# Kernel tuning notes

Measured on AMD Instinct MI355X. Metric: run time of the kernel, lower is better.

Reference implementation:

```python
import math
import jax, jax.numpy as jnp
import numpy as np

D_MODEL = 1024
N_HEADS = 16
HEAD_DIM = D_MODEL // N_HEADS
FEATURE_DIM = 16
WINDOW = 64
EPS_NORM = 1e-6
EPS_DEN = 1e-6

_TRIU_I, _TRIU_J = np.triu_indices(FEATURE_DIM)

def taylor_feature_map(x):
    # x: [B,T,H,f] -> [B,T,H,1+f+f(f+1)/2]
    B, T, H, d = x.shape
    ones = jnp.ones((B, T, H, 1), dtype=x.dtype)
    outer = jnp.einsum('bthd,bthe->bthde', x, x)
    scale = jnp.full((d, d), 1.0 / math.sqrt(2), dtype=x.dtype)
    scale = scale.at[jnp.arange(d), jnp.arange(d)].set(0.5)
    outer = outer * scale
    quadratic = outer[..., _TRIU_I, _TRIU_J]
    return jnp.concatenate([ones, x, quadratic], axis=-1)

def rmsnorm(x, w):
    var = jnp.mean(x * x, axis=-1, keepdims=True)
    return x * jax.lax.rsqrt(var + EPS_NORM) * w

def setup_inputs() -> dict:
    key = jax.random.key(0)
    ks = jax.random.split(key, 9)
    B, T = 2, 2048
    std = 0.02
    return {
        'x': jax.random.normal(ks[0], (B, T, D_MODEL), jnp.float32),
        'encoder_out': jax.random.normal(ks[1], (B, T, D_MODEL), jnp.float32),
        'norm_w': jnp.ones((D_MODEL,), jnp.float32),
        'Wq': jax.random.normal(ks[2], (D_MODEL, D_MODEL), jnp.float32) * std,
        'Wkv': jax.random.normal(ks[3], (D_MODEL, 2 * D_MODEL), jnp.float32) * std,
        'Wqf': jax.random.normal(ks[4], (HEAD_DIM, FEATURE_DIM), jnp.float32) * std,
        'Wkf': jax.random.normal(ks[5], (HEAD_DIM, FEATURE_DIM), jnp.float32) * std,
        'Wwin': jax.random.normal(ks[6], (D_MODEL, 2 * D_MODEL), jnp.float32) * std,
        'Wout': jax.random.normal(ks[7], (2 * D_MODEL, D_MODEL), jnp.float32) * std,
    }

def _forward(x, encoder_out, norm_w, Wq, Wkv, Wqf, Wkf, Wwin, Wout):
    residual = x
    xn = rmsnorm(x, norm_w)
    B, T_dec, _ = xn.shape
    T_enc = encoder_out.shape[1]
    H, hd = N_HEADS, HEAD_DIM

    q = (xn @ Wq).reshape(B, T_dec, H, hd)
    kv = (encoder_out @ Wkv).reshape(B, T_enc, 2, H, hd)
    k, v = kv[:, :, 0], kv[:, :, 1]

    # Taylor linear cross-attention
    q_phi = taylor_feature_map(q @ Wqf)   # [B,T_dec,H,F]
    k_phi = taylor_feature_map(k @ Wkf)   # [B,T_enc,H,F]
    kv_state = jnp.einsum('bshf,bshd->bhfd', k_phi, v)
    k_state = k_phi.sum(axis=1)           # [B,H,F]
    linear_out = jnp.einsum('bthf,bhfd->bthd', q_phi, kv_state)
    normalizer = jnp.einsum('bthf,bhf->bth', q_phi, k_state)[..., None]
    linear_out = (linear_out / (normalizer + EPS_DEN)).reshape(B, T_dec, D_MODEL)

    # Sliding-window causal self-attention (flash window_size=(WINDOW,0))
    kv_win = (xn @ Wwin).reshape(B, T_dec, 2, H, hd)
    k_win, v_win = kv_win[:, :, 0], kv_win[:, :, 1]
    scores = jnp.einsum('bthd,bshd->bhts', q, k_win) * (1.0 / math.sqrt(hd))
    i = jnp.arange(T_dec)[:, None]
    j = jnp.arange(T_dec)[None, :]
    allowed = (j <= i) & (j >= i - WINDOW)
    scores = jnp.where(allowed, scores, jnp.finfo(scores.dtype).min)
    probs = jax.nn.softmax(scores, axis=-1)
    window_out = jnp.einsum('bhts,bshd->bthd', probs, v_win).reshape(B, T_dec, D_MODEL)

    combined = jnp.concatenate([linear_out, window_out], axis=-1)
    return residual + combined @ Wout

def reference(x, encoder_out, norm_w, Wq, Wkv, Wqf, Wkf, Wwin, Wout):
    return _forward(x, encoder_out, norm_w, Wq, Wkv, Wqf, Wkf, Wwin, Wout)
```

## Files before the change

kernel.cpp:

```cpp
#include <hip/hip_runtime.h>

#define DM 1024
#define NH 16
#define HD 64
#define FD 16
#define NF 153
#define FPAD 160
#define WIN 64
#define TSEQ 2048
#define ROWS 4096
#define KSPLIT 8
#define RS2 0.70710678118654752f

typedef unsigned short u16;
typedef __attribute__((ext_vector_type(8))) short bf16x8;
typedef __attribute__((ext_vector_type(8))) unsigned short u16x8;
typedef __attribute__((ext_vector_type(4))) unsigned short u16x4;
typedef __attribute__((ext_vector_type(4))) float f32x4;

#define GLB_AS __attribute__((address_space(1)))
#define LDS_AS __attribute__((address_space(3)))

static __device__ __forceinline__ void gload_lds16(const void* g, void* l){
  __builtin_amdgcn_global_load_lds((const GLB_AS void*)g, (LDS_AS void*)l, 16, 0, 0);
}

static __device__ __forceinline__ float bf2f(u16 u){
  unsigned v = ((unsigned)u) << 16;
  return __builtin_bit_cast(float, v);
}
static __device__ __forceinline__ u16 f2bf(float f){
  unsigned u = __builtin_bit_cast(unsigned, f);
  u += 0x7FFFu + ((u >> 16) & 1u);
  return (u16)(u >> 16);
}

static __device__ __forceinline__ void tr_tile(const float* __restrict__ in,
    u16* __restrict__ out, int K, int N, int n0, int k0, float* t, int tid){
  int tx = tid & 31, ty = tid >> 5;
  #pragma unroll
  for (int i=0;i<4;i++) t[(ty + i*8)*33 + tx] = in[(size_t)(k0 + ty + i*8)*N + n0 + tx];
  __syncthreads();
  #pragma unroll
  for (int i=0;i<4;i++) out[(size_t)(n0 + ty + i*8)*K + k0 + tx] = f2bf(t[tx*33 + ty + i*8]);
}

__global__ __launch_bounds__(256) void k_prep(const float* __restrict__ x,
    const float* __restrict__ enc, const float* __restrict__ w,
    const float* __restrict__ Wq, const float* __restrict__ Wwin,
    const float* __restrict__ Wkv, const float* __restrict__ Wout,
    const float* __restrict__ Wqf, const float* __restrict__ Wkf,
    u16* __restrict__ xn, u16* __restrict__ encb,
    u16* __restrict__ WqwT, u16* __restrict__ WkvT, u16* __restrict__ WoutT,
    u16* __restrict__ WqfT, u16* __restrict__ WkfT){
  __shared__ float t[32*33];
  int bx = blockIdx.x, tid = threadIdx.x;
  if (bx < ROWS){
    int row = bx;
    const float4* xr = (const float4*)(x + (size_t)row*DM);
    float4 a = xr[tid];
    float ss = a.x*a.x + a.y*a.y + a.z*a.z + a.w*a.w;
    #pragma unroll
    for (int m=1;m<64;m<<=1) ss += __shfl_xor(ss, m);
    __shared__ float red[4];
    if ((tid&63)==0) red[tid>>6] = ss;
    __syncthreads();
    float tot = red[0]+red[1]+red[2]+red[3];
    float rs = rsqrtf(tot*(1.0f/DM) + 1e-6f);
    float4 wv = ((const float4*)w)[tid];
    u16x4 o;
    o[0]=f2bf(a.x*rs*wv.x); o[1]=f2bf(a.y*rs*wv.y);
    o[2]=f2bf(a.z*rs*wv.z); o[3]=f2bf(a.w*rs*wv.w);
    ((u16x4*)(xn + (size_t)row*DM))[tid] = o;
  } else if (bx < 2*ROWS){
    int row = bx - ROWS;
    float4 a = ((const float4*)(enc + (size_t)row*DM))[tid];
    u16x4 o;
    o[0]=f2bf(a.x); o[1]=f2bf(a.y); o[2]=f2bf(a.z); o[3]=f2bf(a.w);
    ((u16x4*)(encb + (size_t)row*DM))[tid] = o;
  } else {
    int b = bx - 2*ROWS;
    if (b < 1024){
      tr_tile(Wq, WqwT, 1024, 1024, (b&31)*32, (b>>5)*32, t, tid);
    } else if (b < 3072){
      int r = b-1024;
      tr_tile(Wwin, WqwT + (size_t)1024*1024, 1024, 2048, (r&63)*32, (r>>6)*32, t, tid);
    } else if (b < 5120){
      int r = b-3072;
      tr_tile(Wkv, WkvT, 1024, 2048, (r&63)*32, (r>>6)*32, t, tid);
    } else if (b < 7168){
      int r = b-5120;
      tr_tile(Wout, WoutT, 2048, 1024, (r&31)*32, (r>>5)*32, t, tid);
    } else {
      const float* src = (b==7168) ? Wqf : Wkf;
      u16* dst = (b==7168) ? WqfT : WkfT;
      for (int i=tid;i<1024;i+=256) dst[i] = f2bf(src[(i&63)*16 + (i>>6)]);
    }
  }
}

template<int EPI>
__global__ __launch_bounds__(512) void k_gemm(
    const u16* __restrict__ A0, const u16* __restrict__ B0, u16* __restrict__ C0, int ldc0,
    const u16* __restrict__ A1, const u16* __restrict__ B1, u16* __restrict__ C1, int ldc1,
    int split, int K, float* __restrict__ Cf, const float* __restrict__ resid){
  __shared__ u16 As0[128*64];
  __shared__ u16 Bs0[128*64];
  __shared__ u16 As1[128*64];
  __shared__ u16 Bs1[128*64];
  int by = blockIdx.y;
  const u16 *A, *Bt; u16* C; int ldc;
  if (by < split){ A=A0; Bt=B0; C=C0; ldc=ldc0; }
  else { by -= split; A=A1; Bt=B1; C=C1; ldc=ldc1; }
  int row0 = blockIdx.x*128, col0 = by*128;
  int tid = threadIdx.x, lane = tid&63, wid = tid>>6;
  int wm = wid>>2, wn = wid&3;
  int srow = lane>>3;
  int scb  = ((lane&7)*16) ^ (srow<<4);
  f32x4 acc[4][2] = {};

  auto STAGE = [&](u16* Asb, u16* Bsb, int k0){
    #pragma unroll
    for (int i=0;i<2;i++){
      int chunk = wid*2 + i;
      int r = chunk*8 + srow;
      gload_lds16((const char*)(A  + (size_t)(row0+r)*K + k0) + scb, (char*)Asb + chunk*1024);
      gload_lds16((const char*)(Bt + (size_t)(col0+r)*K + k0) + scb, (char*)Bsb + chunk*1024);
    }
  };
  auto COMPUTE = [&](const u16* Asb, const u16* Bsb){
    #pragma unroll
    for (int kk=0;kk<64;kk+=32){
      int bc = 2*(kk + ((lane>>4)<<3));
      bf16x8 af[4], bfm[2];
      #pragma unroll
      for (int m=0;m<4;m++){
        int r = wm*64 + m*16 + (lane&15);
        af[m]  = *(const bf16x8*)((const char*)Asb + r*128 + (bc ^ ((r&7)<<4)));
      }
      #pragma unroll
      for (int n=0;n<2;n++){
        int r = wn*32 + n*16 + (lane&15);
        bfm[n] = *(const bf16x8*)((const char*)Bsb + r*128 + (bc ^ ((r&7)<<4)));
      }
      #pragma unroll
      for (int m=0;m<4;m++)
        #pragma unroll
        for (int n=0;n<2;n++)
          acc[m][n] = __builtin_amdgcn_mfma_f32_16x16x32_bf16(af[m], bfm[n], acc[m][n], 0,0,0);
    }
  };

  int nt = K >> 6;
  STAGE(As0, Bs0, 0);
  for (int t=0; t<nt-2; t+=2){
    STAGE(As1, Bs1, (t+1)*64);
    asm volatile("s_waitcnt vmcnt(4)" ::: "memory");
    __builtin_amdgcn_s_barrier();
    COMPUTE(As0, Bs0);
    __builtin_amdgcn_s_barrier();
    STAGE(As0, Bs0, (t+2)*64);
    asm volatile("s_waitcnt vmcnt(4)" ::: "memory");
    __builtin_amdgcn_s_barrier();
    COMPUTE(As1, Bs1);
    __builtin_amdgcn_s_barrier();
  }
  STAGE(As1, Bs1, (nt-1)*64);
  asm volatile("s_waitcnt vmcnt(4)" ::: "memory");
  __builtin_amdgcn_s_barrier();
  COMPUTE(As0, Bs0);
  asm volatile("s_waitcnt vmcnt(0)" ::: "memory");
  __builtin_amdgcn_s_barrier();
  COMPUTE(As1, Bs1);

  int rl = (lane>>4)<<2;
  #pragma unroll
  for (int m=0;m<4;m++){
    #pragma unroll
    for (int n=0;n<2;n++){
      int gc = col0 + wn*32 + n*16 + (lane&15);
      #pragma unroll
      for (int r=0;r<4;r++){
        size_t gi = (size_t)(row0 + wm*64 + m*16 + rl + r)*ldc + gc;
        if constexpr (EPI) Cf[gi] = acc[m][n][r] + resid[gi];
        else               C[gi]  = f2bf(acc[m][n][r]);
      }
    }
  }
}

__global__ __launch_bounds__(256) void k_kvstate(const u16* __restrict__ kvb,
    const u16* __restrict__ WkfT, float* __restrict__ part){
  const int P = 76;
  __shared__ u16 kc[64*64];
  __shared__ u16 wb[16*72];
  __shared__ float fL[64*16];
  __shared__ u16 ph[160*P];
  __shared__ u16 vt[80*P];
  int bh = blockIdx.x, b = bh>>4, h = bh&15;
  int ks = blockIdx.y;
  int tid = threadIdx.x, lane = tid&63, w = tid>>6;
  int srow = lane>>3;
  int scb  = ((lane&7)*16) ^ (srow<<4);
  for (int i=tid;i<1024;i+=256) wb[(i>>6)*72 + (i&63)] = WkfT[i];
  for (int i=tid; i<16*P; i+=256){
    int r = 64 + i/P, c = i - (i/P)*P;
    vt[r*P + c] = (r==64) ? (u16)0x3F80 : (u16)0;
  }
  f32x4 acc[5][3] = {};
  for (int c=0;c<4;c++){
    int s0 = ks*256 + c*64;
    __syncthreads();
    #pragma unroll
    for (int i=0;i<2;i++){
      int ch = w + i*4;
      int r = ch*8 + srow;
      gload_lds16((const char*)(kvb + (size_t)(b*TSEQ + s0 + r)*2048 + h*HD) + scb,
                  (char*)kc + ch*1024);
    }
    for (int s = w; s < 64; s += 4)
      vt[lane*P + s] = kvb[(size_t)(b*TSEQ + s0 + s)*2048 + 1024 + h*HD + lane];
    __syncthreads();
    {
      f32x4 fa = {};
      #pragma unroll
      for (int kk=0;kk<2;kk++){
        int bc = 2*(kk*32 + ((lane>>4)<<3));
        int r = w*16 + (lane&15);
        bf16x8 av = *(const bf16x8*)((const char*)kc + r*128 + (bc ^ ((r&7)<<4)));
        bf16x8 bv = *(const bf16x8*)(wb + (lane&15)*72 + kk*32 + ((lane>>4)<<3));
        fa = __builtin_amdgcn_mfma_f32_16x16x32_bf16(av, bv, fa, 0,0,0);
      }
      int rl = (lane>>4)<<2;
      #pragma unroll
      for (int r=0;r<4;r++) fL[(w*16 + rl + r)*16 + (lane&15)] = fa[r];
    }
    __syncthreads();
    {
      int r = tid>>2, jq = tid&3;
      float4 v0 = *(const float4*)(fL + r*16 + 0);
      float4 v1 = *(const float4*)(fL + r*16 + 4);
      float4 v2 = *(const float4*)(fL + r*16 + 8);
      float4 v3 = *(const float4*)(fL + r*16 + 12);
      float f[16] = {v0.x,v0.y,v0.z,v0.w, v1.x,v1.y,v1.z,v1.w,
                     v2.x,v2.y,v2.z,v2.w, v3.x,v3.y,v3.z,v3.w};
      if ((0&3)==jq) ph[0*P + r] = 0x3F80;
      #pragma unroll
      for (int q=0;q<16;q++) if (((1+q)&3)==jq) ph[(1+q)*P + r] = f2bf(f[q]);
      int pos = 17;
      #pragma unroll
      for (int i=0;i<16;i++)
        #pragma unroll
        for (int j=i;j<16;j++){
          if ((pos&3)==jq) ph[pos*P + r] = f2bf(f[i]*f[j]*((i==j)?0.5f:RS2));
          pos++;
        }
      #pragma unroll
      for (int z=153;z<160;z++) if ((z&3)==jq) ph[z*P + r] = 0;
    }
    __syncthreads();
    #pragma unroll
    for (int kk=0;kk<2;kk++){
      int lk = kk*32 + ((lane>>4)<<3);
      bf16x8 bfr[3];
      #pragma unroll
      for (int nn=0;nn<3;nn++){
        int ncol = (nn<2) ? (w*2+nn) : (8+(w&1));
        bfr[nn] = *(const bf16x8*)(ph + (ncol*16 + (lane&15))*P + lk);
      }
      #pragma unroll
      for (int m=0;m<5;m++){
        bf16x8 av = *(const bf16x8*)(vt + (m*16 + (lane&15))*P + lk);
        #pragma unroll
        for (int nn=0;nn<3;nn++)
          acc[m][nn] = __builtin_amdgcn_mfma_f32_16x16x32_bf16(av, bfr[nn], acc[m][nn], 0,0,0);
      }
    }
  }
  int rl = (lane>>4)<<2;
  float* pp = part + ((size_t)ks*32 + bh)*80*160;
  #pragma unroll
  for (int m=0;m<5;m++){
    #pragma unroll
    for (int nn=0;nn<3;nn++){
      int ncol = (nn<2) ? (w*2+nn) : (8+(w&1));
      if (nn==2 && w>=2) continue;
      int fcol = ncol*16 + (lane&15);
      #pragma unroll
      for (int r=0;r<4;r++)
        pp[(size_t)(m*16 + rl + r)*160 + fcol] = acc[m][nn][r];
    }
  }
}

__global__ __launch_bounds__(256) void k_kvreduce(const float* __restrict__ part,
    u16* __restrict__ kvsT){
  int i = blockIdx.x*256 + threadIdx.x;
  float s = 0.f;
  #pragma unroll
  for (int c=0;c<KSPLIT;c++) s += part[(size_t)c*409600 + i];
  kvsT[i] = f2bf(s);
}

__global__ __launch_bounds__(256) void k_linattn(const u16* __restrict__ qwin,
    const u16* __restrict__ WqfT, const u16* __restrict__ kvsT, u16* __restrict__ comb){
  const int LS = 168;
  __shared__ u16 As[64*LS];
  __shared__ u16 Bs[80*LS];
  __shared__ u16 qc[64*64];
  __shared__ u16 wb[16*72];
  __shared__ float fL[64*16];
  int bh = blockIdx.x, b = bh>>4, h = bh&15;
  int t0 = blockIdx.y*64;
  int tid = threadIdx.x, lane = tid&63, wid = tid>>6;
  int srow = lane>>3;
  int scb  = ((lane&7)*16) ^ (srow<<4);
  for (int i=tid;i<1024;i+=256) wb[(i>>6)*72 + (i&63)] = WqfT[i];
  for (int i=tid*8; i<80*FPAD; i+=2048){
    int r = i/FPAD, ff = i - r*FPAD;
    *(bf16x8*)(Bs + r*LS + ff) = *(const bf16x8*)(kvsT + (size_t)bh*80*FPAD + i);
  }
  #pragma unroll
  for (int i=0;i<2;i++){
    int ch = wid + i*4;
    int r = ch*8 + srow;
    gload_lds16((const char*)(qwin + (size_t)(b*TSEQ + t0 + r)*3072 + h*HD) + scb,
                (char*)qc + ch*1024);
  }
  __syncthreads();
  {
    f32x4 fa = {};
    #pragma unroll
    for (int kk=0;kk<2;kk++){
      int bc = 2*(kk*32 + ((lane>>4)<<3));
      int r = wid*16 + (lane&15);
      bf16x8 av = *(const bf16x8*)((const char*)qc + r*128 + (bc ^ ((r&7)<<4)));
      bf16x8 bv = *(const bf16x8*)(wb + (lane&15)*72 + kk*32 + ((lane>>4)<<3));
      fa = __builtin_amdgcn_mfma_f32_16x16x32_bf16(av, bv, fa, 0,0,0);
    }
    int rl = (lane>>4)<<2;
    #pragma unroll
    for (int r=0;r<4;r++) fL[(wid*16 + rl + r)*16 + (lane&15)] = fa[r];
  }
  __syncthreads();
  {
    int r = tid>>2, jq = tid&3;
    float4 v0 = *(const float4*)(fL + r*16 + 0);
    float4 v1 = *(const float4*)(fL + r*16 + 4);
    float4 v2 = *(const float4*)(fL + r*16 + 8);
    float4 v3 = *(const float4*)(fL + r*16 + 12);
    float f[16] = {v0.x,v0.y,v0.z,v0.w, v1.x,v1.y,v1.z,v1.w,
                   v2.x,v2.y,v2.z,v2.w, v3.x,v3.y,v3.z,v3.w};
    if ((0&3)==jq) As[r*LS + 0] = 0x3F80;
    #pragma unroll
    for (int q=0;q<16;q++) if (((1+q)&3)==jq) As[r*LS + 1+q] = f2bf(f[q]);
    int pos = 17;
    #pragma unroll
    for (int i=0;i<16;i++)
      #pragma unroll
      for (int j=i;j<16;j++){
        if ((pos&3)==jq) As[r*LS + pos] = f2bf(f[i]*f[j]*((i==j)?0.5f:RS2));
        pos++;
      }
    #pragma unroll
    for (int z=153;z<160;z++) if ((z&3)==jq) As[r*LS + z] = 0;
  }
  __syncthreads();
  f32x4 acc[5] = {};
  #pragma unroll
  for (int ks=0;ks<5;ks++){
    int lk = ks*32 + ((lane>>4)<<3);
    bf16x8 a = *(const bf16x8*)(As + (wid*16 + (lane&15))*LS + lk);
    #pragma unroll
    for (int n=0;n<5;n++){
      bf16x8 bb = *(const bf16x8*)(Bs + (n*16 + (lane&15))*LS + lk);
      acc[n] = __builtin_amdgcn_mfma_f32_16x16x32_bf16(a, bb, acc[n], 0,0,0);
    }
  }
  int rl = (lane>>4)<<2;
  #pragma unroll
  for (int r=0;r<4;r++){
    float nrm = __shfl(acc[4][r], lane & 48) + 1e-6f;
    float inv = 1.0f / nrm;
    int t = t0 + wid*16 + rl + r;
    #pragma unroll
    for (int n=0;n<4;n++){
      comb[(size_t)(b*TSEQ + t)*2048 + h*64 + n*16 + (lane&15)] = f2bf(acc[n][r]*inv);
    }
  }
}

__global__ __launch_bounds__(256) void k_window(const u16* __restrict__ q, int ldq,
    const u16* __restrict__ kvwin, int ldkv, u16* __restrict__ comb){
  const int LQ = 72, LV = 136;
  __shared__ u16 q_s [64*LQ];
  __shared__ u16 k_s [128*LQ];
  __shared__ u16 vT_s[64*LV];
  __shared__ u16 p_s [64*LV];
  int bh = blockIdx.x, b = bh>>4, h = bh&15;
  int t0 = blockIdx.y*64;
  int tid = threadIdx.x, lane = tid&63, wid = tid>>6;
  int j0 = t0 - 64;
  bf16x8 zv = {0,0,0,0,0,0,0,0};
  for (int cc=tid; cc<512; cc+=256){
    int r = cc>>3, c8 = cc&7;
    *(bf16x8*)(q_s + r*LQ + c8*8) =
      *(const bf16x8*)(q + (size_t)(b*TSEQ + t0 + r)*ldq + h*HD + c8*8);
  }
  for (int cc=tid; cc<1024; cc+=256){
    int r = cc>>3, c8 = cc&7;
    int j = j0 + r;
    bf16x8 kv8 = (j>=0) ? *(const bf16x8*)(kvwin + (size_t)(b*TSEQ + j)*ldkv + h*HD + c8*8) : zv;
    *(bf16x8*)(k_s + r*LQ + c8*8) = kv8;
    bf16x8 vv8 = (j>=0) ? *(const bf16x8*)(kvwin + (size_t)(b*TSEQ + j)*ldkv + 1024 + h*HD + c8*8) : zv;
    #pragma unroll
    for (int e=0;e<8;e++) vT_s[(c8*8+e)*LV + r] = (u16)vv8[e];
  }
  __syncthreads();
  f32x4 sa[8] = {};
  #pragma unroll
  for (int kk=0;kk<64;kk+=32){
    int lk = kk + ((lane>>4)<<3);
    bf16x8 a = *(const bf16x8*)(q_s + (wid*16 + (lane&15))*LQ + lk);
    #pragma unroll
    for (int n=0;n<8;n++){
      bf16x8 bb = *(const bf16x8*)(k_s + (n*16 + (lane&15))*LQ + lk);
      sa[n] = __builtin_amdgcn_mfma_f32_16x16x32_bf16(a, bb, sa[n], 0,0,0);
    }
  }
  int rl = (lane>>4)<<2;
  float pr[8][4];
  #pragma unroll
  for (int r=0;r<4;r++){
    int ig = t0 + wid*16 + rl + r;
    float mx = -1e30f;
    float sv[8];
    #pragma unroll
    for (int n=0;n<8;n++){
      int jg = j0 + n*16 + (lane&15);
      float s = sa[n][r]*0.125f;
      bool ok = (jg>=0) && (jg<=ig) && (jg>=ig-WIN);
      s = ok ? s : -1e30f;
      sv[n]=s; mx = fmaxf(mx, s);
    }
    #pragma unroll
    for (int m=1;m<16;m<<=1) mx = fmaxf(mx, __shfl_xor(mx, m));
    float sum = 0.f;
    #pragma unroll
    for (int n=0;n<8;n++){ float e = __expf(sv[n]-mx); sv[n]=e; sum += e; }
    #pragma unroll
    for (int m=1;m<16;m<<=1) sum += __shfl_xor(sum, m);
    float inv = 1.0f/sum;
    #pragma unroll
    for (int n=0;n<8;n++) pr[n][r] = sv[n]*inv;
  }
  #pragma unroll
  for (int n=0;n<8;n++)
    #pragma unroll
    for (int r=0;r<4;r++)
      p_s[(wid*16 + rl + r)*LV + n*16 + (lane&15)] = f2bf(pr[n][r]);
  __syncthreads();
  f32x4 oa[4] = {};
  #pragma unroll
  for (int ks=0;ks<4;ks++){
    int lk = ks*32 + ((lane>>4)<<3);
    bf16x8 a = *(const bf16x8*)(p_s + (wid*16 + (lane&15))*LV + lk);
    #pragma unroll
    for (int n=0;n<4;n++){
      bf16x8 bb = *(const bf16x8*)(vT_s + (n*16 + (lane&15))*LV + lk);
      oa[n] = __builtin_amdgcn_mfma_f32_16x16x32_bf16(a, bb, oa[n], 0,0,0);
    }
  }
  #pragma unroll
  for (int n=0;n<4;n++)
    #pragma unroll
    for (int r=0;r<4;r++)
      comb[(size_t)(b*TSEQ + t0 + wid*16 + rl + r)*2048 + 1024 + h*HD + n*16 + (lane&15)]
        = f2bf(oa[n][r]);
}

extern "C" void kernel_launch(void* const* d_in, const int* in_sizes, int n_in,
                              void* d_out, int out_size, void* d_ws, size_t ws_size,
                              hipStream_t stream){
  (void)in_sizes; (void)n_in; (void)out_size; (void)ws_size;
  const float* x    = (const float*)d_in[0];
  const float* enc  = (const float*)d_in[1];
  const float* nw   = (const float*)d_in[2];
  const float* Wq   = (const float*)d_in[3];
  const float* Wkv  = (const float*)d_in[4];
  const float* Wqf  = (const float*)d_in[5];
  const float* Wkf  = (const float*)d_in[6];
  const float* Wwin = (const float*)d_in[7];
  const float* Wout = (const float*)d_in[8];
  float* out = (float*)d_out;

  char* p = (char*)d_ws;
  auto alloc = [&](size_t bytes)->char*{
    char* r = p; p += (bytes + 255) & ~(size_t)255; return r;
  };
  char*  aliasBase = p;
  u16*   xn    = (u16*)  alloc((size_t)ROWS*DM*2);
  u16*   encb  = (u16*)  alloc((size_t)ROWS*DM*2);
  u16*   WqwT  = (u16*)  alloc((size_t)3072*DM*2);
  u16*   WkvT  = (u16*)  alloc((size_t)2048*DM*2);
  float* part  = (float*)aliasBase;
  u16*   WoutT = (u16*)  alloc((size_t)DM*2048*2);
  u16*   WqfT  = (u16*)  alloc((size_t)FD*HD*2);
  u16*   WkfT  = (u16*)  alloc((size_t)FD*HD*2);
  u16*   qwin  = (u16*)  alloc((size_t)ROWS*3072*2);
  u16*   kvb   = (u16*)  alloc((size_t)ROWS*2048*2);
  u16*   kvsT  = (u16*)  alloc((size_t)32*80*FPAD*2);
  u16*   comb  = (u16*)  alloc((size_t)ROWS*2048*2);

  k_prep<<<2*ROWS + 7170, 256, 0, stream>>>(x, enc, nw, Wq, Wwin, Wkv, Wout, Wqf, Wkf,
                                            xn, encb, WqwT, WkvT, WoutT, WqfT, WkfT);

  k_gemm<0><<<dim3(ROWS/128, 40), 512, 0, stream>>>(
      xn, WqwT, qwin, 3072,  encb, WkvT, kvb, 2048,  24, DM, nullptr, nullptr);

  k_kvstate<<<dim3(32, KSPLIT), 256, 0, stream>>>(kvb, WkfT, part);
  k_kvreduce<<<1600, 256, 0, stream>>>(part, kvsT);

  k_linattn<<<dim3(32, TSEQ/64), 256, 0, stream>>>(qwin, WqfT, kvsT, comb);
  k_window <<<dim3(32, TSEQ/64), 256, 0, stream>>>(qwin, 3072, qwin + 1024, 3072, comb);

  k_gemm<1><<<dim3(ROWS/128, 8), 512, 0, stream>>>(
      comb, WoutT, nullptr, DM,  nullptr, nullptr, nullptr, 0,  8, 2048, out, x);
}
```

Before: 162.8 us.

## Fuse linear and window attention kernels; use 64-row tiles for output GEMM

Merges the Taylor linear-attention kernel and the sliding-window attention kernel into one k_attn kernel. The fused kernel loads the q tile once and shares an LDS arena between phases, which saves one launch and one reload of q. The output projection GEMM moves to a new 64x128-tile, 256-thread kernel, doubling the block count for 4096x1024 so more CUs are busy. Risks are lower per-block operand reuse in the GEMM and a longer serial dependency chain inside the fused attention block.

```diff
diff --git a/kernel.cpp b/kernel.cpp
--- a/kernel.cpp
+++ b/kernel.cpp
@@ -189,6 +189,96 @@
   }
 }
 
+template<int EPI>
+__global__ __launch_bounds__(256) void k_gemm64(const u16* __restrict__ A,
+    const u16* __restrict__ Bt, u16* __restrict__ C, float* __restrict__ Cf,
+    const float* __restrict__ resid, int ldc, int K){
+  __shared__ u16 As0[64*64];
+  __shared__ u16 Bs0[128*64];
+  __shared__ u16 As1[64*64];
+  __shared__ u16 Bs1[128*64];
+  int row0 = blockIdx.x*64, col0 = blockIdx.y*128;
+  int tid = threadIdx.x, lane = tid&63, wid = tid>>6;
+  int wm = wid>>1, wn = wid&1;
+  int srow = lane>>3;
+  int scb  = ((lane&7)*16) ^ (srow<<4);
+  f32x4 acc[2][4] = {};
+
+  auto STAGE = [&](u16* Asb, u16* Bsb, int k0){
+    #pragma unroll
+    for (int j=0;j<2;j++){
+      int c = wid*2 + j;
+      int r = c*8 + srow;
+      gload_lds16((const char*)(A + (size_t)(row0+r)*K + k0) + scb, (char*)Asb + c*1024);
+    }
+    #pragma unroll
+    for (int j=0;j<4;j++){
+      int c = wid*4 + j;
+      int r = c*8 + srow;
+      gload_lds16((const char*)(Bt + (size_t)(col0+r)*K + k0) + scb, (char*)Bsb + c*1024);
+    }
+  };
+  auto COMPUTE = [&](const u16* Asb, const u16* Bsb){
+    #pragma unroll
+    for (int kk=0;kk<64;kk+=32){
+      int bc = 2*(kk + ((lane>>4)<<3));
+      bf16x8 af[2], bfm[4];
+      #pragma unroll
+      for (int m=0;m<2;m++){
+        int r = wm*32 + m*16 + (lane&15);
+        af[m]  = *(const bf16x8*)((const char*)Asb + r*128 + (bc ^ ((r&7)<<4)));
+      }
+      #pragma unroll
+      for (int n=0;n<4;n++){
+        int r = wn*64 + n*16 + (lane&15);
+        bfm[n] = *(const bf16x8*)((const char*)Bsb + r*128 + (bc ^ ((r&7)<<4)));
+      }
+      #pragma unroll
+      for (int m=0;m<2;m++)
+        #pragma unroll
+        for (int n=0;n<4;n++)
+          acc[m][n] = __builtin_amdgcn_mfma_f32_16x16x32_bf16(af[m], bfm[n], acc[m][n], 0,0,0);
+    }
+  };
+
+  int nt = K >> 6;
+  STAGE(As0, Bs0, 0);
+  for (int t=0; t<nt-2; t+=2){
+    STAGE(As1, Bs1, (t+1)*64);
+    asm volatile("s_waitcnt vmcnt(6)" ::: "memory");
+    __builtin_amdgcn_s_barrier();
+    COMPUTE(As0, Bs0);
+    __builtin_amdgcn_s_barrier();
+    STAGE(As0, Bs0, (t+2)*64);
+    asm volatile("s_waitcnt vmcnt(6)" ::: "memory");
+    __builtin_amdgcn_s_barrier();
+    COMPUTE(As1, Bs1);
+    __builtin_amdgcn_s_barrier();
+  }
+  STAGE(As1, Bs1, (nt-1)*64);
+  asm volatile("s_waitcnt vmcnt(6)" ::: "memory");
+  __builtin_amdgcn_s_barrier();
+  COMPUTE(As0, Bs0);
+  asm volatile("s_waitcnt vmcnt(0)" ::: "memory");
+  __builtin_amdgcn_s_barrier();
+  COMPUTE(As1, Bs1);
+
+  int rl = (lane>>4)<<2;
+  #pragma unroll
+  for (int m=0;m<2;m++){
+    #pragma unroll
+    for (int n=0;n<4;n++){
+      int gc = col0 + wn*64 + n*16 + (lane&15);
+      #pragma unroll
+      for (int r=0;r<4;r++){
+        size_t gi = (size_t)(row0 + wm*32 + m*16 + rl + r)*ldc + gc;
+        if constexpr (EPI) Cf[gi] = acc[m][n][r] + resid[gi];
+        else               C[gi]  = f2bf(acc[m][n][r]);
+      }
+    }
+  }
+}
+
 __global__ __launch_bounds__(256) void k_kvstate(const u16* __restrict__ kvb,
     const u16* __restrict__ WkfT, float* __restrict__ part){
   const int P = 76;
@@ -302,24 +392,26 @@
   kvsT[i] = f2bf(s);
 }
 
-__global__ __launch_bounds__(256) void k_linattn(const u16* __restrict__ qwin,
+__global__ __launch_bounds__(256) void k_attn(const u16* __restrict__ qwin,
     const u16* __restrict__ WqfT, const u16* __restrict__ kvsT, u16* __restrict__ comb){
-  const int LS = 168;
-  __shared__ u16 As[64*LS];
-  __shared__ u16 Bs[80*LS];
-  __shared__ u16 qc[64*64];
-  __shared__ u16 wb[16*72];
-  __shared__ float fL[64*16];
+  const int LS = 168, LQ = 72, LV = 136;
+  __shared__ u16 arena[4096 + 1152 + 26624];
+  u16*   qc  = arena;
+  u16*   wb  = arena + 4096;
+  u16*   uni = arena + 5248;
+  float* fL  = (float*)uni;
+  u16*   As  = uni + 2048;
+  u16*   Bs  = uni + 12800;
+  u16*   k_s = uni;
+  u16*   vT  = uni + 9216;
+  u16*   p_s = uni + 17920;
+
   int bh = blockIdx.x, b = bh>>4, h = bh&15;
   int t0 = blockIdx.y*64;
   int tid = threadIdx.x, lane = tid&63, wid = tid>>6;
   int srow = lane>>3;
   int scb  = ((lane&7)*16) ^ (srow<<4);
-  for (int i=tid;i<1024;i+=256) wb[(i>>6)*72 + (i&63)] = WqfT[i];
-  for (int i=tid*8; i<80*FPAD; i+=2048){
-    int r = i/FPAD, ff = i - r*FPAD;
-    *(bf16x8*)(Bs + r*LS + ff) = *(const bf16x8*)(kvsT + (size_t)bh*80*FPAD + i);
-  }
+
   #pragma unroll
   for (int i=0;i<2;i++){
     int ch = wid + i*4;
@@ -327,7 +419,13 @@
     gload_lds16((const char*)(qwin + (size_t)(b*TSEQ + t0 + r)*3072 + h*HD) + scb,
                 (char*)qc + ch*1024);
   }
+  for (int i=tid;i<1024;i+=256) wb[(i>>6)*72 + (i&63)] = WqfT[i];
+  for (int i=tid*8; i<80*FPAD; i+=2048){
+    int r = i/FPAD, ff = i - r*FPAD;
+    *(bf16x8*)(Bs + r*LS + ff) = *(const bf16x8*)(kvsT + (size_t)bh*80*FPAD + i);
+  }
   __syncthreads();
+
   {
     f32x4 fa = {};
     #pragma unroll
@@ -343,6 +441,7 @@
     for (int r=0;r<4;r++) fL[(wid*16 + rl + r)*16 + (lane&15)] = fa[r];
   }
   __syncthreads();
+
   {
     int r = tid>>2, jq = tid&3;
     float4 v0 = *(const float4*)(fL + r*16 + 0);
@@ -366,62 +465,53 @@
     for (int z=153;z<160;z++) if ((z&3)==jq) As[r*LS + z] = 0;
   }
   __syncthreads();
-  f32x4 acc[5] = {};
-  #pragma unroll
-  for (int ks=0;ks<5;ks++){
-    int lk = ks*32 + ((lane>>4)<<3);
-    bf16x8 a = *(const bf16x8*)(As + (wid*16 + (lane&15))*LS + lk);
-    #pragma unroll
-    for (int n=0;n<5;n++){
-      bf16x8 bb = *(const bf16x8*)(Bs + (n*16 + (lane&15))*LS + lk);
-      acc[n] = __builtin_amdgcn_mfma_f32_16x16x32_bf16(a, bb, acc[n], 0,0,0);
-    }
-  }
-  int rl = (lane>>4)<<2;
-  #pragma unroll
-  for (int r=0;r<4;r++){
-    float nrm = __shfl(acc[4][r], lane & 48) + 1e-6f;
-    float inv = 1.0f / nrm;
-    int t = t0 + wid*16 + rl + r;
-    #pragma unroll
-    for (int n=0;n<4;n++){
-      comb[(size_t)(b*TSEQ + t)*2048 + h*64 + n*16 + (lane&15)] = f2bf(acc[n][r]*inv);
-    }
-  }
-}
-
-__global__ __launch_bounds__(256) void k_window(const u16* __restrict__ q, int ldq,
-    const u16* __restrict__ kvwin, int ldkv, u16* __restrict__ comb){
-  const int LQ = 72, LV = 136;
-  __shared__ u16 q_s [64*LQ];
-  __shared__ u16 k_s [128*LQ];
-  __shared__ u16 vT_s[64*LV];
-  __shared__ u16 p_s [64*LV];
-  int bh = blockIdx.x, b = bh>>4, h = bh&15;
-  int t0 = blockIdx.y*64;
-  int tid = threadIdx.x, lane = tid&63, wid = tid>>6;
+
+  {
+    f32x4 acc[5] = {};
+    #pragma unroll
+    for (int ks=0;ks<5;ks++){
+      int lk = ks*32 + ((lane>>4)<<3);
+      bf16x8 a = *(const bf16x8*)(As + (wid*16 + (lane&15))*LS + lk);
+      #pragma unroll
+      for (int n=0;n<5;n++){
+        bf16x8 bb = *(const bf16x8*)(Bs + (n*16 + (lane&15))*LS + lk);
+        acc[n] = __builtin_amdgcn_mfma_f32_16x16x32_bf16(a, bb, acc[n], 0,0,0);
+      }
+    }
+    int rl = (lane>>4)<<2;
+    #pragma unroll
+    for (int r=0;r<4;r++){
+      float nrm = __shfl(acc[4][r], lane & 48) + 1e-6f;
+      float inv = 1.0f / nrm;
+      int t = t0 + wid*16 + rl + r;
+      #pragma unroll
+      for (int n=0;n<4;n++){
+        comb[(size_t)(b*TSEQ + t)*2048 + h*64 + n*16 + (lane&15)] = f2bf(acc[n][r]*inv);
+      }
+    }
+  }
+  __syncthreads();
+
   int j0 = t0 - 64;
   bf16x8 zv = {0,0,0,0,0,0,0,0};
-  for (int cc=tid; cc<512; cc+=256){
-    int r = cc>>3, c8 = cc&7;
-    *(bf16x8*)(q_s + r*LQ + c8*8) =
-      *(const bf16x8*)(q + (size_t)(b*TSEQ + t0 + r)*ldq + h*HD + c8*8);
-  }
   for (int cc=tid; cc<1024; cc+=256){
     int r = cc>>3, c8 = cc&7;
     int j = j0 + r;
-    bf16x8 kv8 = (j>=0) ? *(const bf16x8*)(kvwin + (size_t)(b*TSEQ + j)*ldkv + h*HD + c8*8) : zv;
+    bf16x8 kv8 = (j>=0) ? *(const bf16x8*)(qwin + (size_t)(b*TSEQ + j)*3072 + 1024 + h*HD + c8*8) : zv;
     *(bf16x8*)(k_s + r*LQ + c8*8) = kv8;
-    bf16x8 vv8 = (j>=0) ? *(const bf16x8*)(kvwin + (size_t)(b*TSEQ + j)*ldkv + 1024 + h*HD + c8*8) : zv;
-    #pragma unroll
-    for (int e=0;e<8;e++) vT_s[(c8*8+e)*LV + r] = (u16)vv8[e];
+    bf16x8 vv8 = (j>=0) ? *(const bf16x8*)(qwin + (size_t)(b*TSEQ + j)*3072 + 2048 + h*HD + c8*8) : zv;
+    #pragma unroll
+    for (int e=0;e<8;e++) vT[(c8*8+e)*LV + r] = (u16)vv8[e];
   }
   __syncthreads();
+
   f32x4 sa[8] = {};
   #pragma unroll
   for (int kk=0;kk<64;kk+=32){
+    int bc = 2*(kk + ((lane>>4)<<3));
+    int rq = wid*16 + (lane&15);
+    bf16x8 a = *(const bf16x8*)((const char*)qc + rq*128 + (bc ^ ((rq&7)<<4)));
     int lk = kk + ((lane>>4)<<3);
-    bf16x8 a = *(const bf16x8*)(q_s + (wid*16 + (lane&15))*LQ + lk);
     #pragma unroll
     for (int n=0;n<8;n++){
       bf16x8 bb = *(const bf16x8*)(k_s + (n*16 + (lane&15))*LQ + lk);
@@ -460,6 +550,7 @@
     for (int r=0;r<4;r++)
       p_s[(wid*16 + rl + r)*LV + n*16 + (lane&15)] = f2bf(pr[n][r]);
   __syncthreads();
+
   f32x4 oa[4] = {};
   #pragma unroll
   for (int ks=0;ks<4;ks++){
@@ -467,7 +558,7 @@
     bf16x8 a = *(const bf16x8*)(p_s + (wid*16 + (lane&15))*LV + lk);
     #pragma unroll
     for (int n=0;n<4;n++){
-      bf16x8 bb = *(const bf16x8*)(vT_s + (n*16 + (lane&15))*LV + lk);
+      bf16x8 bb = *(const bf16x8*)(vT + (n*16 + (lane&15))*LV + lk);
       oa[n] = __builtin_amdgcn_mfma_f32_16x16x32_bf16(a, bb, oa[n], 0,0,0);
     }
   }
@@ -521,9 +612,8 @@
   k_kvstate<<<dim3(32, KSPLIT), 256, 0, stream>>>(kvb, WkfT, part);
   k_kvreduce<<<1600, 256, 0, stream>>>(part, kvsT);
 
-  k_linattn<<<dim3(32, TSEQ/64), 256, 0, stream>>>(qwin, WqfT, kvsT, comb);
-  k_window <<<dim3(32, TSEQ/64), 256, 0, stream>>>(qwin, 3072, qwin + 1024, 3072, comb);
-
-  k_gemm<1><<<dim3(ROWS/128, 8), 512, 0, stream>>>(
-      comb, WoutT, nullptr, DM,  nullptr, nullptr, nullptr, 0,  8, 2048, out, x);
-}
+  k_attn<<<dim3(32, TSEQ/64), 256, 0, stream>>>(qwin, WqfT, kvsT, comb);
+
+  k_gemm64<1><<<dim3(ROWS/64, 8), 256, 0, stream>>>(
+      comb, WoutT, nullptr, out, x, DM, 2048);
+}
```

Measured after the change: 159.9 us. Within noise of the previous version (-1.7%).
